# Kernel tuning notes

Measured on AMD Instinct MI355X. Metric: run time of the kernel, lower is better.

## Reference

```python
import jax, jax.numpy as jnp
import numpy as np

# ---- constants from init_kwargs ----
TAU_MEM = 10.0
TAU_SYN = np.array([5.0, 2.0], dtype=np.float32)
THRESHOLD = 1.0
WINDOW = 0.3
BATCH = 32
T = 1024
N_NEURONS = 1024
N_SYN = len(TAU_SYN)

def _bitshift(tau):
    b = np.round(np.log2(np.asarray(tau, dtype=np.float32)))
    return np.maximum(b, 0.0).astype(np.float32)

DASH_MEM = float(_bitshift(TAU_MEM))          # 3.0 -> decay factor 2^-3
DASH_SYN = _bitshift(TAU_SYN)                  # [2.0, 1.0]
MEM_DECAY = np.float32(2.0 ** (-DASH_MEM))     # fraction removed per step
SYN_DECAY = (2.0 ** (-DASH_SYN)).astype(np.float32)  # (n_syn,)


def setup_inputs() -> dict:
    key = jax.random.key(0)
    # Bernoulli spike raster, (batch*T, n_syn, n_neurons)
    u = jax.random.uniform(key, (BATCH * T, N_SYN, N_NEURONS), dtype=jnp.float32)
    binary_input = (u < 0.2).astype(jnp.float32)
    return {"binary_input": binary_input}


def _lif_scan(syn_out):
    """syn_out: (T, B, N, n_syn). Bitshift-decay LIF with membrane-subtract reset."""
    syn_decay = jnp.asarray(SYN_DECAY)  # (n_syn,)
    mem_decay = jnp.float32(MEM_DECAY)
    vmem0 = jnp.zeros((BATCH, N_NEURONS), jnp.float32)
    isyn0 = jnp.zeros((BATCH, N_NEURONS, N_SYN), jnp.float32)

    def step(carry, inp_t):
        vmem, isyn = carry
        # bitshift decay: x -= x >> dash  <=>  x -= x * 2^-dash
        isyn = isyn - isyn * syn_decay + inp_t            # (B, N, n_syn)
        vmem = vmem - vmem * mem_decay + isyn.sum(-1)     # (B, N)
        spk = (vmem >= THRESHOLD).astype(vmem.dtype)
        vmem = vmem - spk * THRESHOLD                     # membrane subtract
        return (vmem, isyn), (spk, vmem)

    (_, _), (spikes, vmem_rec) = jax.lax.scan(step, (vmem0, isyn0), syn_out)
    return spikes, vmem_rec  # (T, B, N) each


def reference(binary_input):
    # (B*T, n_syn, N) -> (B, T, n_syn, N) -> (T, B, n_syn, N) -> (T, B, N, n_syn)
    x = binary_input.reshape(BATCH, T, N_SYN, N_NEURONS)
    x = jnp.swapaxes(x, 0, 1)
    x = jnp.moveaxis(x, -2, -1)
    spikes, _ = _lif_scan(x)
    # (T, B, N) -> (B, T, N) -> (B*T, N)
    out = jnp.swapaxes(spikes, 0, 1).reshape(BATCH * T, N_NEURONS)
    return out
```

## Files before the change

kernel.cpp:

```cpp
#include <hip/hip_runtime.h>
#include <stdint.h>


#define TT 1024
#define NN 1024
#define BB 32
#define UU 16

__global__ __launch_bounds__(64, 1)
void lif_scan_kernel(const float* __restrict__ in, float* __restrict__ out) {
    __shared__ float sbuf[2][UU][2][64];

    const int lane = threadIdx.x;
    const int b  = blockIdx.x >> 4;
    const int n0 = (blockIdx.x & 15) << 6;

    const float* gin  = in  + (size_t)b * TT * 2 * NN + n0 + lane;
    float*       gout = out + (size_t)b * TT * NN     + n0 + lane;

    const float SD0 = 0.25f;
    const float SD1 = 0.5f;
    const float MD  = 0.125f;

    float i0 = 0.0f, i1 = 0.0f, v = 0.0f;

#pragma unroll
    for (int j = 0; j < UU; ++j) {
#pragma unroll
        for (int s = 0; s < 2; ++s) {
            __builtin_amdgcn_global_load_lds(
                (const float __attribute__((address_space(1)))*)(gin + j * 2048 + s * 1024),
                (float __attribute__((address_space(3)))*)(&sbuf[0][j][s][0]),
                4, 0, 0);
        }
    }
    __builtin_amdgcn_s_waitcnt(0x0F70);
    asm volatile("" ::: "memory");

    int p = 0;
    for (int tc = 0; tc < TT; tc += UU, p ^= 1) {
        if (tc + UU < TT) {
            const float* gnext = gin + (size_t)(tc + UU) * 2048;
#pragma unroll
            for (int j = 0; j < UU; ++j) {
#pragma unroll
                for (int s = 0; s < 2; ++s) {
                    __builtin_amdgcn_global_load_lds(
                        (const float __attribute__((address_space(1)))*)(gnext + j * 2048 + s * 1024),
                        (float __attribute__((address_space(3)))*)(&sbuf[p ^ 1][j][s][0]),
                        4, 0, 0);
                }
            }
        }

        float spk[UU];
#pragma unroll
        for (int j = 0; j < UU; ++j) {
            float x0 = sbuf[p][j][0][lane];
            float x1 = sbuf[p][j][1][lane];
            i0 = (i0 - i0 * SD0) + x0;
            i1 = (i1 - i1 * SD1) + x1;
            float vd = v - v * MD;
            v = vd + (i0 + i1);
            float s_ = (v >= 1.0f) ? 1.0f : 0.0f;
            v -= s_;
            spk[j] = s_;
        }

        __builtin_amdgcn_s_waitcnt(0x0F70);
        asm volatile("" ::: "memory");

        float* go = gout + (size_t)tc * NN;
#pragma unroll
        for (int j = 0; j < UU; ++j) go[j * NN] = spk[j];
    }
}

extern "C" void kernel_launch(void* const* d_in, const int* in_sizes, int n_in,
                              void* d_out, int out_size, void* d_ws, size_t ws_size,
                              hipStream_t stream) {
    const float* in = (const float*)d_in[0];
    float* out = (float*)d_out;
    dim3 grid(BB * NN / 64);
    dim3 block(64);
    hipLaunchKernelGGL(lif_scan_kernel, grid, block, 0, stream, in, out);
}
```

Before: 393.4 us.

## Warp-specialize LIF scan with three loader waves feeding one compute wave

Splits each block into one compute wave and three producer waves. The producers load the next chunk of 32 timesteps from global memory through registers into a double-buffered LDS tile, and block-wide barriers hand each chunk over. This replaces the single wave's async global-to-LDS loads and waitcnt, and aims to put more loads in flight per CU while the serial recurrence runs. The cost is four times the threads per block, a barrier on every chunk, and an extra register-to-LDS store step.

```diff
diff --git a/kernel.cpp b/kernel.cpp
--- a/kernel.cpp
+++ b/kernel.cpp
@@ -1,78 +1,97 @@
 #include <hip/hip_runtime.h>
-#include <stdint.h>
 
 
 #define TT 1024
 #define NN 1024
 #define BB 32
-#define UU 16
+#define CH 32
+#define NCH (TT / CH)
+#define NROW (CH * 2)
 
-__global__ __launch_bounds__(64, 1)
+__global__ __launch_bounds__(256, 1)
 void lif_scan_kernel(const float* __restrict__ in, float* __restrict__ out) {
-    __shared__ float sbuf[2][UU][2][64];
+    __shared__ float sbuf[2][CH][2][64];
 
-    const int lane = threadIdx.x;
-    const int b  = blockIdx.x >> 4;
-    const int n0 = (blockIdx.x & 15) << 6;
+    const int tid  = threadIdx.x;
+    const int wave = tid >> 6;
+    const int lane = tid & 63;
+    const int b    = blockIdx.x >> 4;
+    const int n0   = (blockIdx.x & 15) << 6;
 
-    const float* gin  = in  + (size_t)b * TT * 2 * NN + n0 + lane;
-    float*       gout = out + (size_t)b * TT * NN     + n0 + lane;
+    const float* gin  = in  + (size_t)b * TT * 2 * NN + n0;
+    float*       gout = out + (size_t)b * TT * NN     + n0;
 
-    const float SD0 = 0.25f;
-    const float SD1 = 0.5f;
-    const float MD  = 0.125f;
+    if (wave == 0) {
+        const float SD0 = 0.25f;
+        const float SD1 = 0.5f;
+        const float MD  = 0.125f;
+        float i0 = 0.0f, i1 = 0.0f, v = 0.0f;
+        float spk[CH];
 
-    float i0 = 0.0f, i1 = 0.0f, v = 0.0f;
+        __syncthreads();
 
+        for (int c = 0; c < NCH; ++c) {
+            if (c > 0) {
+                float* go = gout + (size_t)(c - 1) * CH * NN + lane;
 #pragma unroll
-    for (int j = 0; j < UU; ++j) {
+                for (int j = 0; j < CH; ++j) go[j * NN] = spk[j];
+            }
+            const int p = c & 1;
 #pragma unroll
-        for (int s = 0; s < 2; ++s) {
-            __builtin_amdgcn_global_load_lds(
-                (const float __attribute__((address_space(1)))*)(gin + j * 2048 + s * 1024),
-                (float __attribute__((address_space(3)))*)(&sbuf[0][j][s][0]),
-                4, 0, 0);
+            for (int j = 0; j < CH; ++j) {
+                float x0 = sbuf[p][j][0][lane];
+                float x1 = sbuf[p][j][1][lane];
+                i0 = (i0 - i0 * SD0) + x0;
+                i1 = (i1 - i1 * SD1) + x1;
+                float vd = v - v * MD;
+                v = vd + (i0 + i1);
+                float s_ = (v >= 1.0f) ? 1.0f : 0.0f;
+                v -= s_;
+                spk[j] = s_;
+            }
+            __syncthreads();
         }
-    }
-    __builtin_amdgcn_s_waitcnt(0x0F70);
-    asm volatile("" ::: "memory");
+        float* go = gout + (size_t)(NCH - 1) * CH * NN + lane;
+#pragma unroll
+        for (int j = 0; j < CH; ++j) go[j * NN] = spk[j];
 
-    int p = 0;
-    for (int tc = 0; tc < TT; tc += UU, p ^= 1) {
-        if (tc + UU < TT) {
-            const float* gnext = gin + (size_t)(tc + UU) * 2048;
+    } else {
+        const int li = wave - 1;
+        float vbuf[22];
+
+        {
 #pragma unroll
-            for (int j = 0; j < UU; ++j) {
+            for (int m = 0; m < 22; ++m) {
+                int r = m * 3 + li;
+                if (r < NROW)
+                    vbuf[m] = gin[(size_t)(r >> 1) * 2048 + (r & 1) * 1024 + lane];
+            }
 #pragma unroll
-                for (int s = 0; s < 2; ++s) {
-                    __builtin_amdgcn_global_load_lds(
-                        (const float __attribute__((address_space(1)))*)(gnext + j * 2048 + s * 1024),
-                        (float __attribute__((address_space(3)))*)(&sbuf[p ^ 1][j][s][0]),
-                        4, 0, 0);
+            for (int m = 0; m < 22; ++m) {
+                int r = m * 3 + li;
+                if (r < NROW) sbuf[0][r >> 1][r & 1][lane] = vbuf[m];
+            }
+        }
+        __syncthreads();
+
+        for (int c = 0; c < NCH; ++c) {
+            if (c + 1 < NCH) {
+                const float* gc = gin + (size_t)(c + 1) * CH * 2048;
+                const int p = (c + 1) & 1;
+#pragma unroll
+                for (int m = 0; m < 22; ++m) {
+                    int r = m * 3 + li;
+                    if (r < NROW)
+                        vbuf[m] = gc[(size_t)(r >> 1) * 2048 + (r & 1) * 1024 + lane];
+                }
+#pragma unroll
+                for (int m = 0; m < 22; ++m) {
+                    int r = m * 3 + li;
+                    if (r < NROW) sbuf[p][r >> 1][r & 1][lane] = vbuf[m];
                 }
             }
+            __syncthreads();
         }
-
-        float spk[UU];
-#pragma unroll
-        for (int j = 0; j < UU; ++j) {
-            float x0 = sbuf[p][j][0][lane];
-            float x1 = sbuf[p][j][1][lane];
-            i0 = (i0 - i0 * SD0) + x0;
-            i1 = (i1 - i1 * SD1) + x1;
-            float vd = v - v * MD;
-            v = vd + (i0 + i1);
-            float s_ = (v >= 1.0f) ? 1.0f : 0.0f;
-            v -= s_;
-            spk[j] = s_;
-        }
-
-        __builtin_amdgcn_s_waitcnt(0x0F70);
-        asm volatile("" ::: "memory");
-
-        float* go = gout + (size_t)tc * NN;
-#pragma unroll
-        for (int j = 0; j < UU; ++j) go[j * NN] = spk[j];
     }
 }
 
@@ -82,6 +101,6 @@
     const float* in = (const float*)d_in[0];
     float* out = (float*)d_out;
     dim3 grid(BB * NN / 64);
-    dim3 block(64);
+    dim3 block(256);
     hipLaunchKernelGGL(lif_scan_kernel, grid, block, 0, stream, in, out);
 }
```

Result: slower. 401.3 us (+2.0%).
